# Kernel optimization log

Measured on AMD Instinct MI355X. Metric: run time of the kernel, lower is better.

## Reference

```python
import jax, jax.numpy as jnp
import numpy as np

B = 16384

def setup_inputs() -> dict:
    key = jax.random.key(0)
    ks = jax.random.split(key, 10)
    def lin(kw, fan_in, fan_out):
        lim = 1.0 / np.sqrt(fan_in)
        k1, k2 = jax.random.split(kw)
        w = jax.random.uniform(k1, (fan_out, fan_in), jnp.float32, -lim, lim)
        b = jax.random.uniform(k2, (fan_out,), jnp.float32, -lim, lim)
        return w, b
    x = jax.random.normal(ks[0], (B, 784), dtype=jnp.float32)
    conv_w = jnp.ones((3, 3), dtype=jnp.float32)
    w1, b1 = lin(ks[1], 676, 256)
    w2, b2 = lin(ks[2], 256, 128)
    w3, b3 = lin(ks[3], 128, 64)
    w4, b4 = lin(ks[4], 64, 10)
    return {"x": x, "conv_w": conv_w, "w1": w1, "b1": b1, "w2": w2, "b2": b2,
            "w3": w3, "b3": b3, "w4": w4, "b4": b4}

def reference(x, conv_w, w1, b1, w2, b2, w3, b3, w4, b4):
    b = x.shape[0]
    img = x.reshape(b, 1, 28, 28)                      # NCHW
    kern = conv_w.reshape(1, 1, 3, 3)                   # OIHW
    conv = jax.lax.conv_general_dilated(
        img, kern, window_strides=(1, 1), padding='VALID',
        dimension_numbers=('NCHW', 'OIHW', 'NCHW'))     # [B,1,26,26]
    h = conv.reshape(b, 26 * 26)
    h1 = jax.nn.relu(h @ w1.T + b1)
    h2 = jax.nn.relu(h1 @ w2.T + b2)
    h3 = jax.nn.relu(h2 @ w3.T + b3)
    out = h3 @ w4.T + b4                                # [B,10] logits
    return out
```

## Files before the change

### kernel.cpp

```cpp
#include <hip/hip_runtime.h>
#include <hip/hip_bf16.h>

typedef __attribute__((ext_vector_type(8))) short bf16x8;
typedef __attribute__((ext_vector_type(4))) float f32x4;

__device__ __forceinline__ unsigned short f2bf(float f) {
  unsigned int u = __builtin_bit_cast(unsigned int, f);
  u += 0x7fffu + ((u >> 16) & 1u);
  return (unsigned short)(u >> 16);
}

__device__ __forceinline__ f32x4 mfma16(bf16x8 a, bf16x8 b, f32x4 c) {
  return __builtin_amdgcn_mfma_f32_16x16x32_bf16(a, b, c, 0, 0, 0);
}

__global__ void prep_weights(const float* __restrict__ w1, const float* __restrict__ w2,
                             const float* __restrict__ w3, const float* __restrict__ w4,
                             unsigned short* __restrict__ w1b, unsigned short* __restrict__ w2b,
                             unsigned short* __restrict__ w3b, unsigned short* __restrict__ w4b) {
  const int idx = blockIdx.x * blockDim.x + threadIdx.x;
  const int stride = gridDim.x * blockDim.x;
  for (int i = idx; i < 256 * 704; i += stride) {
    int o = i / 704, k = i - o * 704;
    w1b[i] = f2bf(k < 676 ? w1[o * 676 + k] : 0.f);
  }
  for (int i = idx; i < 128 * 256; i += stride) w2b[i] = f2bf(w2[i]);
  for (int i = idx; i < 64 * 128; i += stride) w3b[i] = f2bf(w3[i]);
  for (int i = idx; i < 16 * 64; i += stride) {
    int o = i >> 6, k = i & 63;
    w4b[i] = f2bf(o < 10 ? w4[o * 64 + k] : 0.f);
  }
}

__global__ __launch_bounds__(256, 2) void fused_mlp(
    const float* __restrict__ x,
    const float* __restrict__ cw,
    const unsigned short* __restrict__ w1b,
    const unsigned short* __restrict__ w2b,
    const unsigned short* __restrict__ w3b,
    const unsigned short* __restrict__ w4b,
    const float* __restrict__ b1, const float* __restrict__ b2,
    const float* __restrict__ b3, const float* __restrict__ b4,
    float* __restrict__ out)
{
  __shared__ unsigned short lds_s[22784];
  unsigned short* hbT = lds_s;
  unsigned short* h1s = lds_s;
  unsigned short* h2s = lds_s + 8448;
  unsigned short* h3s = lds_s + 12800;

  const int tid = threadIdx.x;
  const int lane = tid & 63;
  const int lane15 = lane & 15;
  const int kg = (lane >> 4) << 3;
  const int w = tid >> 6;
  const int row0 = blockIdx.x * 32;
  const int rb = (lane >> 4) << 2;

  {
    const float c0 = cw[0], c1 = cw[1], c2 = cw[2];
    const float c3 = cw[3], c4 = cw[4], c5 = cw[5];
    const float c6 = cw[6], c7 = cw[7], c8 = cw[8];
    const float* xblk = x + (size_t)row0 * 784;
    for (int f = tid; f < 32 * 182; f += 256) {
      int rr = f / 182;
      int t = f - rr * 182;
      int i = t / 7;
      int jq = t - i * 7;
      int j0 = jq << 2;
      const float* xr = xblk + rr * 784 + i * 28 + j0;
      if (jq < 6) {
        float4 v00 = *(const float4*)(xr);
        float4 v01 = *(const float4*)(xr + 4);
        float4 v10 = *(const float4*)(xr + 28);
        float4 v11 = *(const float4*)(xr + 32);
        float4 v20 = *(const float4*)(xr + 56);
        float4 v21 = *(const float4*)(xr + 60);
        float r0[8] = {v00.x, v00.y, v00.z, v00.w, v01.x, v01.y, v01.z, v01.w};
        float r1[8] = {v10.x, v10.y, v10.z, v10.w, v11.x, v11.y, v11.z, v11.w};
        float r2[8] = {v20.x, v20.y, v20.z, v20.w, v21.x, v21.y, v21.z, v21.w};
        float o[4];
#pragma unroll
        for (int tt = 0; tt < 4; ++tt) {
          o[tt] = c0 * r0[tt] + c1 * r0[tt + 1] + c2 * r0[tt + 2]
                + c3 * r1[tt] + c4 * r1[tt + 1] + c5 * r1[tt + 2]
                + c6 * r2[tt] + c7 * r2[tt + 1] + c8 * r2[tt + 2];
        }
        unsigned int p0 = (unsigned)f2bf(o[0]) | ((unsigned)f2bf(o[1]) << 16);
        unsigned int p1 = (unsigned)f2bf(o[2]) | ((unsigned)f2bf(o[3]) << 16);
        unsigned int* dst = (unsigned int*)(hbT + rr * 712 + i * 26 + j0);
        dst[0] = p0;
        dst[1] = p1;
      } else {
        float4 v0 = *(const float4*)(xr);
        float4 v1 = *(const float4*)(xr + 28);
        float4 v2 = *(const float4*)(xr + 56);
        float o0 = c0 * v0.x + c1 * v0.y + c2 * v0.z
                 + c3 * v1.x + c4 * v1.y + c5 * v1.z
                 + c6 * v2.x + c7 * v2.y + c8 * v2.z;
        float o1 = c0 * v0.y + c1 * v0.z + c2 * v0.w
                 + c3 * v1.y + c4 * v1.z + c5 * v1.w
                 + c6 * v2.y + c7 * v2.z + c8 * v2.w;
        unsigned int p0 = (unsigned)f2bf(o0) | ((unsigned)f2bf(o1) << 16);
        *(unsigned int*)(hbT + rr * 712 + i * 26 + 24) = p0;
      }
    }
    for (int f = tid; f < 32 * 14; f += 256) {
      int rr = f / 14, u = f - rr * 14;
      *(unsigned int*)(hbT + rr * 712 + 676 + (u << 1)) = 0u;
    }
  }

  __syncthreads();

  f32x4 acc1[2][4] = {};
  {
    const unsigned short* a0p = hbT + lane15 * 712 + kg;
    const unsigned short* a1p = hbT + (16 + lane15) * 712 + kg;
    const unsigned short* bp = w1b + (w * 64 + lane15) * 704 + kg;
#pragma unroll 2
    for (int ks = 0; ks < 22; ++ks) {
      const int k0 = ks << 5;
      bf16x8 a0 = *(const bf16x8*)(a0p + k0);
      bf16x8 a1 = *(const bf16x8*)(a1p + k0);
      bf16x8 fb0 = *(const bf16x8*)(bp + k0);
      bf16x8 fb1 = *(const bf16x8*)(bp + 16 * 704 + k0);
      bf16x8 fb2 = *(const bf16x8*)(bp + 32 * 704 + k0);
      bf16x8 fb3 = *(const bf16x8*)(bp + 48 * 704 + k0);
      acc1[0][0] = mfma16(a0, fb0, acc1[0][0]);
      acc1[1][0] = mfma16(a1, fb0, acc1[1][0]);
      acc1[0][1] = mfma16(a0, fb1, acc1[0][1]);
      acc1[1][1] = mfma16(a1, fb1, acc1[1][1]);
      acc1[0][2] = mfma16(a0, fb2, acc1[0][2]);
      acc1[1][2] = mfma16(a1, fb2, acc1[1][2]);
      acc1[0][3] = mfma16(a0, fb3, acc1[0][3]);
      acc1[1][3] = mfma16(a1, fb3, acc1[1][3]);
    }
  }

  __syncthreads();

#pragma unroll
  for (int n = 0; n < 4; ++n) {
    const int col = w * 64 + n * 16 + lane15;
    const float bias = b1[col];
#pragma unroll
    for (int m = 0; m < 2; ++m) {
#pragma unroll
      for (int r = 0; r < 4; ++r) {
        float v = acc1[m][n][r] + bias;
        v = v > 0.f ? v : 0.f;
        h1s[(rb + m * 16 + r) * 264 + col] = f2bf(v);
      }
    }
  }
  __syncthreads();

  f32x4 acc2[2][2] = {};
  {
    const unsigned short* a0p = h1s + lane15 * 264 + kg;
    const unsigned short* a1p = h1s + (16 + lane15) * 264 + kg;
    const unsigned short* bp = w2b + (w * 32 + lane15) * 256 + kg;
#pragma unroll
    for (int ks = 0; ks < 8; ++ks) {
      const int k0 = ks << 5;
      bf16x8 a0 = *(const bf16x8*)(a0p + k0);
      bf16x8 a1 = *(const bf16x8*)(a1p + k0);
      bf16x8 fb0 = *(const bf16x8*)(bp + k0);
      bf16x8 fb1 = *(const bf16x8*)(bp + 16 * 256 + k0);
      acc2[0][0] = mfma16(a0, fb0, acc2[0][0]);
      acc2[1][0] = mfma16(a1, fb0, acc2[1][0]);
      acc2[0][1] = mfma16(a0, fb1, acc2[0][1]);
      acc2[1][1] = mfma16(a1, fb1, acc2[1][1]);
    }
  }
#pragma unroll
  for (int n = 0; n < 2; ++n) {
    const int col = w * 32 + n * 16 + lane15;
    const float bias = b2[col];
#pragma unroll
    for (int m = 0; m < 2; ++m) {
#pragma unroll
      for (int r = 0; r < 4; ++r) {
        float v = acc2[m][n][r] + bias;
        v = v > 0.f ? v : 0.f;
        h2s[(rb + m * 16 + r) * 136 + col] = f2bf(v);
      }
    }
  }
  __syncthreads();

  f32x4 acc3[2] = {};
  {
    const unsigned short* a0p = h2s + lane15 * 136 + kg;
    const unsigned short* a1p = h2s + (16 + lane15) * 136 + kg;
    const unsigned short* bp = w3b + (w * 16 + lane15) * 128 + kg;
#pragma unroll
    for (int ks = 0; ks < 4; ++ks) {
      const int k0 = ks << 5;
      bf16x8 a0 = *(const bf16x8*)(a0p + k0);
      bf16x8 a1 = *(const bf16x8*)(a1p + k0);
      bf16x8 fb0 = *(const bf16x8*)(bp + k0);
      acc3[0] = mfma16(a0, fb0, acc3[0]);
      acc3[1] = mfma16(a1, fb0, acc3[1]);
    }
  }
  {
    const int col = w * 16 + lane15;
    const float bias = b3[col];
#pragma unroll
    for (int m = 0; m < 2; ++m) {
#pragma unroll
      for (int r = 0; r < 4; ++r) {
        float v = acc3[m][r] + bias;
        v = v > 0.f ? v : 0.f;
        h3s[(rb + m * 16 + r) * 72 + col] = f2bf(v);
      }
    }
  }
  __syncthreads();

  if (w < 2) {
    f32x4 acc4 = {};
    const unsigned short* ap = h3s + (w * 16 + lane15) * 72 + kg;
    const unsigned short* bp = w4b + lane15 * 64 + kg;
#pragma unroll
    for (int ks = 0; ks < 2; ++ks) {
      const int k0 = ks << 5;
      bf16x8 a0 = *(const bf16x8*)(ap + k0);
      bf16x8 fb0 = *(const bf16x8*)(bp + k0);
      acc4 = mfma16(a0, fb0, acc4);
    }
    const int col = lane15;
    if (col < 10) {
      const float bias = b4[col];
#pragma unroll
      for (int r = 0; r < 4; ++r) {
        out[(size_t)(row0 + w * 16 + rb + r) * 10 + col] = acc4[r] + bias;
      }
    }
  }
}

extern "C" void kernel_launch(void* const* d_in, const int* in_sizes, int n_in,
                              void* d_out, int out_size, void* d_ws, size_t ws_size,
                              hipStream_t stream) {
  const float* x  = (const float*)d_in[0];
  const float* cw = (const float*)d_in[1];
  const float* w1 = (const float*)d_in[2];
  const float* b1 = (const float*)d_in[3];
  const float* w2 = (const float*)d_in[4];
  const float* b2 = (const float*)d_in[5];
  const float* w3 = (const float*)d_in[6];
  const float* b3 = (const float*)d_in[7];
  const float* w4 = (const float*)d_in[8];
  const float* b4 = (const float*)d_in[9];
  float* out = (float*)d_out;

  unsigned short* w1b = (unsigned short*)d_ws;
  unsigned short* w2b = w1b + 256 * 704;
  unsigned short* w3b = w2b + 128 * 256;
  unsigned short* w4b = w3b + 64 * 128;

  hipLaunchKernelGGL(prep_weights, dim3(256), dim3(256), 0, stream,
                     w1, w2, w3, w4, w1b, w2b, w3b, w4b);

  hipLaunchKernelGGL(fused_mlp, dim3(512), dim3(256), 0, stream,
                     x, cw, w1b, w2b, w3b, w4b, b1, b2, b3, b4, out);
}
```

Measured before the change: 140.3 us.

## Fold 3x3 convolution into first-layer weights and widen blocks to 512 threads

The linear 3x3 conv is folded into W1 in the weight-prep kernel, producing an effective 256x784 (padded to 800) weight, so the main kernel only converts raw x to bf16 in LDS and runs a K=800 GEMM. This removes the per-row stencil compute, but layer 1 now does slightly more MFMA work (K=800 instead of 704). Blocks grow to 512 threads with work per wave halved in each layer, and B fragments for layer 1 are software-prefetched two steps ahead. The prep kernel's folding loop does 9 gathers per output element, which adds some time if prep is inside the measured window.

```diff
diff --git a/kernel.cpp b/kernel.cpp
--- a/kernel.cpp
+++ b/kernel.cpp
@@ -16,13 +16,27 @@
 
 __global__ void prep_weights(const float* __restrict__ w1, const float* __restrict__ w2,
                              const float* __restrict__ w3, const float* __restrict__ w4,
-                             unsigned short* __restrict__ w1b, unsigned short* __restrict__ w2b,
+                             const float* __restrict__ cw,
+                             unsigned short* __restrict__ w1p, unsigned short* __restrict__ w2b,
                              unsigned short* __restrict__ w3b, unsigned short* __restrict__ w4b) {
   const int idx = blockIdx.x * blockDim.x + threadIdx.x;
   const int stride = gridDim.x * blockDim.x;
-  for (int i = idx; i < 256 * 704; i += stride) {
-    int o = i / 704, k = i - o * 704;
-    w1b[i] = f2bf(k < 676 ? w1[o * 676 + k] : 0.f);
+  for (int i = idx; i < 256 * 800; i += stride) {
+    int o = i / 800, p = i - o * 800;
+    float acc = 0.f;
+    if (p < 784) {
+      int u = p / 28, v = p - u * 28;
+#pragma unroll
+      for (int a = 0; a < 3; ++a) {
+#pragma unroll
+        for (int b = 0; b < 3; ++b) {
+          int ii = u - a, jj = v - b;
+          if (ii >= 0 && ii < 26 && jj >= 0 && jj < 26)
+            acc += cw[a * 3 + b] * w1[o * 676 + 26 * ii + jj];
+        }
+      }
+    }
+    w1p[i] = f2bf(acc);
   }
   for (int i = idx; i < 128 * 256; i += stride) w2b[i] = f2bf(w2[i]);
   for (int i = idx; i < 64 * 128; i += stride) w3b[i] = f2bf(w3[i]);
@@ -32,10 +46,9 @@
   }
 }
 
-__global__ __launch_bounds__(256, 2) void fused_mlp(
+__global__ __launch_bounds__(512, 4) void fused_mlp(
     const float* __restrict__ x,
-    const float* __restrict__ cw,
-    const unsigned short* __restrict__ w1b,
+    const unsigned short* __restrict__ w1p,
     const unsigned short* __restrict__ w2b,
     const unsigned short* __restrict__ w3b,
     const unsigned short* __restrict__ w4b,
@@ -43,11 +56,11 @@
     const float* __restrict__ b3, const float* __restrict__ b4,
     float* __restrict__ out)
 {
-  __shared__ unsigned short lds_s[22784];
-  unsigned short* hbT = lds_s;
+  __shared__ unsigned short lds_s[25856];
+  unsigned short* xs  = lds_s;
   unsigned short* h1s = lds_s;
-  unsigned short* h2s = lds_s + 8448;
-  unsigned short* h3s = lds_s + 12800;
+  unsigned short* h2s = lds_s + 12800;
+  unsigned short* h3s = lds_s + 20480;
 
   const int tid = threadIdx.x;
   const int lane = tid & 63;
@@ -58,91 +71,53 @@
   const int rb = (lane >> 4) << 2;
 
   {
-    const float c0 = cw[0], c1 = cw[1], c2 = cw[2];
-    const float c3 = cw[3], c4 = cw[4], c5 = cw[5];
-    const float c6 = cw[6], c7 = cw[7], c8 = cw[8];
     const float* xblk = x + (size_t)row0 * 784;
-    for (int f = tid; f < 32 * 182; f += 256) {
-      int rr = f / 182;
-      int t = f - rr * 182;
-      int i = t / 7;
-      int jq = t - i * 7;
-      int j0 = jq << 2;
-      const float* xr = xblk + rr * 784 + i * 28 + j0;
-      if (jq < 6) {
-        float4 v00 = *(const float4*)(xr);
-        float4 v01 = *(const float4*)(xr + 4);
-        float4 v10 = *(const float4*)(xr + 28);
-        float4 v11 = *(const float4*)(xr + 32);
-        float4 v20 = *(const float4*)(xr + 56);
-        float4 v21 = *(const float4*)(xr + 60);
-        float r0[8] = {v00.x, v00.y, v00.z, v00.w, v01.x, v01.y, v01.z, v01.w};
-        float r1[8] = {v10.x, v10.y, v10.z, v10.w, v11.x, v11.y, v11.z, v11.w};
-        float r2[8] = {v20.x, v20.y, v20.z, v20.w, v21.x, v21.y, v21.z, v21.w};
-        float o[4];
-#pragma unroll
-        for (int tt = 0; tt < 4; ++tt) {
-          o[tt] = c0 * r0[tt] + c1 * r0[tt + 1] + c2 * r0[tt + 2]
-                + c3 * r1[tt] + c4 * r1[tt + 1] + c5 * r1[tt + 2]
-                + c6 * r2[tt] + c7 * r2[tt + 1] + c8 * r2[tt + 2];
-        }
-        unsigned int p0 = (unsigned)f2bf(o[0]) | ((unsigned)f2bf(o[1]) << 16);
-        unsigned int p1 = (unsigned)f2bf(o[2]) | ((unsigned)f2bf(o[3]) << 16);
-        unsigned int* dst = (unsigned int*)(hbT + rr * 712 + i * 26 + j0);
-        dst[0] = p0;
-        dst[1] = p1;
-      } else {
-        float4 v0 = *(const float4*)(xr);
-        float4 v1 = *(const float4*)(xr + 28);
-        float4 v2 = *(const float4*)(xr + 56);
-        float o0 = c0 * v0.x + c1 * v0.y + c2 * v0.z
-                 + c3 * v1.x + c4 * v1.y + c5 * v1.z
-                 + c6 * v2.x + c7 * v2.y + c8 * v2.z;
-        float o1 = c0 * v0.y + c1 * v0.z + c2 * v0.w
-                 + c3 * v1.y + c4 * v1.z + c5 * v1.w
-                 + c6 * v2.y + c7 * v2.z + c8 * v2.w;
-        unsigned int p0 = (unsigned)f2bf(o0) | ((unsigned)f2bf(o1) << 16);
-        *(unsigned int*)(hbT + rr * 712 + i * 26 + 24) = p0;
-      }
-    }
-    for (int f = tid; f < 32 * 14; f += 256) {
-      int rr = f / 14, u = f - rr * 14;
-      *(unsigned int*)(hbT + rr * 712 + 676 + (u << 1)) = 0u;
-    }
-  }
-
-  __syncthreads();
-
-  f32x4 acc1[2][4] = {};
-  {
-    const unsigned short* a0p = hbT + lane15 * 712 + kg;
-    const unsigned short* a1p = hbT + (16 + lane15) * 712 + kg;
-    const unsigned short* bp = w1b + (w * 64 + lane15) * 704 + kg;
-#pragma unroll 2
-    for (int ks = 0; ks < 22; ++ks) {
-      const int k0 = ks << 5;
-      bf16x8 a0 = *(const bf16x8*)(a0p + k0);
-      bf16x8 a1 = *(const bf16x8*)(a1p + k0);
-      bf16x8 fb0 = *(const bf16x8*)(bp + k0);
-      bf16x8 fb1 = *(const bf16x8*)(bp + 16 * 704 + k0);
-      bf16x8 fb2 = *(const bf16x8*)(bp + 32 * 704 + k0);
-      bf16x8 fb3 = *(const bf16x8*)(bp + 48 * 704 + k0);
-      acc1[0][0] = mfma16(a0, fb0, acc1[0][0]);
-      acc1[1][0] = mfma16(a1, fb0, acc1[1][0]);
-      acc1[0][1] = mfma16(a0, fb1, acc1[0][1]);
-      acc1[1][1] = mfma16(a1, fb1, acc1[1][1]);
-      acc1[0][2] = mfma16(a0, fb2, acc1[0][2]);
-      acc1[1][2] = mfma16(a1, fb2, acc1[1][2]);
-      acc1[0][3] = mfma16(a0, fb3, acc1[0][3]);
-      acc1[1][3] = mfma16(a1, fb3, acc1[1][3]);
-    }
-  }
-
-  __syncthreads();
-
-#pragma unroll
-  for (int n = 0; n < 4; ++n) {
-    const int col = w * 64 + n * 16 + lane15;
+    for (int f = tid; f < 32 * 196; f += 512) {
+      int rr = f / 196, c4 = f - rr * 196;
+      float4 v = *(const float4*)(xblk + rr * 784 + (c4 << 2));
+      unsigned int p0 = (unsigned)f2bf(v.x) | ((unsigned)f2bf(v.y) << 16);
+      unsigned int p1 = (unsigned)f2bf(v.z) | ((unsigned)f2bf(v.w) << 16);
+      unsigned int* dst = (unsigned int*)(xs + rr * 808 + (c4 << 2));
+      dst[0] = p0;
+      dst[1] = p1;
+    }
+    if (tid < 256) {
+      int rr = tid >> 3, u = tid & 7;
+      *(unsigned int*)(xs + rr * 808 + 784 + (u << 1)) = 0u;
+    }
+  }
+  __syncthreads();
+
+  f32x4 acc1[2][2] = {};
+  {
+    const unsigned short* a0p = xs + lane15 * 808 + kg;
+    const unsigned short* a1p = xs + (16 + lane15) * 808 + kg;
+    const unsigned short* bp = w1p + (w * 32 + lane15) * 800 + kg;
+    bf16x8 b0a = *(const bf16x8*)(bp);
+    bf16x8 b1a = *(const bf16x8*)(bp + 16 * 800);
+    bf16x8 b0b = *(const bf16x8*)(bp + 32);
+    bf16x8 b1b = *(const bf16x8*)(bp + 16 * 800 + 32);
+#pragma unroll
+    for (int ks = 0; ks < 25; ++ks) {
+      bf16x8 u0 = b0a, u1 = b1a;
+      b0a = b0b; b1a = b1b;
+      if (ks + 2 < 25) {
+        b0b = *(const bf16x8*)(bp + (ks + 2) * 32);
+        b1b = *(const bf16x8*)(bp + 16 * 800 + (ks + 2) * 32);
+      }
+      bf16x8 a0 = *(const bf16x8*)(a0p + ks * 32);
+      bf16x8 a1 = *(const bf16x8*)(a1p + ks * 32);
+      acc1[0][0] = mfma16(a0, u0, acc1[0][0]);
+      acc1[1][0] = mfma16(a1, u0, acc1[1][0]);
+      acc1[0][1] = mfma16(a0, u1, acc1[0][1]);
+      acc1[1][1] = mfma16(a1, u1, acc1[1][1]);
+    }
+  }
+  __syncthreads();
+
+#pragma unroll
+  for (int n = 0; n < 2; ++n) {
+    const int col = w * 32 + n * 16 + lane15;
     const float bias = b1[col];
 #pragma unroll
     for (int m = 0; m < 2; ++m) {
@@ -156,33 +131,29 @@
   }
   __syncthreads();
 
-  f32x4 acc2[2][2] = {};
+  f32x4 acc2[2] = {};
   {
     const unsigned short* a0p = h1s + lane15 * 264 + kg;
     const unsigned short* a1p = h1s + (16 + lane15) * 264 + kg;
-    const unsigned short* bp = w2b + (w * 32 + lane15) * 256 + kg;
+    const unsigned short* bp = w2b + (w * 16 + lane15) * 256 + kg;
 #pragma unroll
     for (int ks = 0; ks < 8; ++ks) {
       const int k0 = ks << 5;
       bf16x8 a0 = *(const bf16x8*)(a0p + k0);
       bf16x8 a1 = *(const bf16x8*)(a1p + k0);
-      bf16x8 fb0 = *(const bf16x8*)(bp + k0);
-      bf16x8 fb1 = *(const bf16x8*)(bp + 16 * 256 + k0);
-      acc2[0][0] = mfma16(a0, fb0, acc2[0][0]);
-      acc2[1][0] = mfma16(a1, fb0, acc2[1][0]);
-      acc2[0][1] = mfma16(a0, fb1, acc2[0][1]);
-      acc2[1][1] = mfma16(a1, fb1, acc2[1][1]);
-    }
-  }
-#pragma unroll
-  for (int n = 0; n < 2; ++n) {
-    const int col = w * 32 + n * 16 + lane15;
+      bf16x8 fb = *(const bf16x8*)(bp + k0);
+      acc2[0] = mfma16(a0, fb, acc2[0]);
+      acc2[1] = mfma16(a1, fb, acc2[1]);
+    }
+  }
+  {
+    const int col = w * 16 + lane15;
     const float bias = b2[col];
 #pragma unroll
     for (int m = 0; m < 2; ++m) {
 #pragma unroll
       for (int r = 0; r < 4; ++r) {
-        float v = acc2[m][n][r] + bias;
+        float v = acc2[m][r] + bias;
         v = v > 0.f ? v : 0.f;
         h2s[(rb + m * 16 + r) * 136 + col] = f2bf(v);
       }
@@ -190,32 +161,25 @@
   }
   __syncthreads();
 
-  f32x4 acc3[2] = {};
-  {
-    const unsigned short* a0p = h2s + lane15 * 136 + kg;
-    const unsigned short* a1p = h2s + (16 + lane15) * 136 + kg;
-    const unsigned short* bp = w3b + (w * 16 + lane15) * 128 + kg;
+  f32x4 acc3 = {};
+  {
+    const int mh = w >> 2, cq = w & 3;
+    const unsigned short* ap = h2s + (mh * 16 + lane15) * 136 + kg;
+    const unsigned short* bp = w3b + (cq * 16 + lane15) * 128 + kg;
 #pragma unroll
     for (int ks = 0; ks < 4; ++ks) {
       const int k0 = ks << 5;
-      bf16x8 a0 = *(const bf16x8*)(a0p + k0);
-      bf16x8 a1 = *(const bf16x8*)(a1p + k0);
-      bf16x8 fb0 = *(const bf16x8*)(bp + k0);
-      acc3[0] = mfma16(a0, fb0, acc3[0]);
-      acc3[1] = mfma16(a1, fb0, acc3[1]);
-    }
-  }
-  {
-    const int col = w * 16 + lane15;
+      bf16x8 a0 = *(const bf16x8*)(ap + k0);
+      bf16x8 fb = *(const bf16x8*)(bp + k0);
+      acc3 = mfma16(a0, fb, acc3);
+    }
+    const int col = cq * 16 + lane15;
     const float bias = b3[col];
 #pragma unroll
-    for (int m = 0; m < 2; ++m) {
-#pragma unroll
-      for (int r = 0; r < 4; ++r) {
-        float v = acc3[m][r] + bias;
-        v = v > 0.f ? v : 0.f;
-        h3s[(rb + m * 16 + r) * 72 + col] = f2bf(v);
-      }
+    for (int r = 0; r < 4; ++r) {
+      float v = acc3[r] + bias;
+      v = v > 0.f ? v : 0.f;
+      h3s[(mh * 16 + rb + r) * 72 + col] = f2bf(v);
     }
   }
   __syncthreads();
@@ -228,8 +192,8 @@
     for (int ks = 0; ks < 2; ++ks) {
       const int k0 = ks << 5;
       bf16x8 a0 = *(const bf16x8*)(ap + k0);
-      bf16x8 fb0 = *(const bf16x8*)(bp + k0);
-      acc4 = mfma16(a0, fb0, acc4);
+      bf16x8 fb = *(const bf16x8*)(bp + k0);
+      acc4 = mfma16(a0, fb, acc4);
     }
     const int col = lane15;
     if (col < 10) {
@@ -257,14 +221,14 @@
   const float* b4 = (const float*)d_in[9];
   float* out = (float*)d_out;
 
-  unsigned short* w1b = (unsigned short*)d_ws;
-  unsigned short* w2b = w1b + 256 * 704;
+  unsigned short* w1p = (unsigned short*)d_ws;
+  unsigned short* w2b = w1p + 256 * 800;
   unsigned short* w3b = w2b + 128 * 256;
   unsigned short* w4b = w3b + 64 * 128;
 
   hipLaunchKernelGGL(prep_weights, dim3(256), dim3(256), 0, stream,
-                     w1, w2, w3, w4, w1b, w2b, w3b, w4b);
-
-  hipLaunchKernelGGL(fused_mlp, dim3(512), dim3(256), 0, stream,
-                     x, cw, w1b, w2b, w3b, w4b, b1, b2, b3, b4, out);
-}
+                     w1, w2, w3, w4, cw, w1p, w2b, w3b, w4b);
+
+  hipLaunchKernelGGL(fused_mlp, dim3(512), dim3(512), 0, stream,
+                     x, w1p, w2b, w3b, w4b, b1, b2, b3, b4, out);
+}
```

New measurement: 125.2 us. 1.12x faster.
